# Optimization experiments

Measured on AMD Instinct MI355X. Metric: run time of the kernel, lower is better.

The kernel has to match this reference:

```python
import jax, jax.numpy as jnp
import numpy as np

# module constants (from init_kwargs)
CS, NV, ED = 8, 4, 32          # codebook_size, num_variables, embedding_dim
VIEWS, D, KSZ = 3, 16, 3        # num_input_channels, depth, kernel_size
HW = 14                         # 7 * scale (scale=2)
CSP = 8                         # spatial of conv_shape after three valid 3x3 convs: 14->12->10->8
KSTATES = CS ** NV              # 4096 combinatorial discrete states


def _elu(x):
    return jnp.where(x > 0, x, jnp.expm1(x))


def _conv_t(x, w, b):
    # PyTorch ConvTranspose2d(stride=1, padding=0); w: (Cin, Cout, k, k)
    wf = jnp.flip(w, (2, 3)).transpose(1, 0, 2, 3)  # -> (Cout, Cin, k, k)
    p = w.shape[2] - 1
    y = jax.lax.conv_general_dilated(x, wf, (1, 1), [(p, p), (p, p)],
                                     dimension_numbers=('NCHW', 'OIHW', 'NCHW'))
    return y + b[None, :, None, None]


def setup_inputs() -> dict:
    key = jax.random.key(0)
    ks = jax.random.split(key, 10)
    rn = lambda k, shape, s=1.0: jax.random.normal(k, shape, jnp.float32) * s
    return {
        'x': rn(ks[0], (64, VIEWS, HW, HW)),
        'latent_embedding': rn(ks[1], (NV, CS, ED)),
        'lin_w': rn(ks[2], (VIEWS, ED * NV, 4 * D * CSP * CSP), 0.05),
        'lin_b': rn(ks[3], (VIEWS, 4 * D * CSP * CSP), 0.05),
        'w1': rn(ks[4], (VIEWS, 4 * D, 2 * D, KSZ, KSZ), 0.05),
        'b1': rn(ks[5], (VIEWS, 2 * D), 0.05),
        'w2': rn(ks[6], (VIEWS, 2 * D, D, KSZ, KSZ), 0.05),
        'b2': rn(ks[7], (VIEWS, D), 0.05),
        'w3': rn(ks[8], (VIEWS, D, 1, KSZ, KSZ), 0.05),
        'b3': rn(ks[9], (VIEWS, 1), 0.05),
    }


def reference(x, latent_embedding, lin_w, lin_b, w1, b1, w2, b2, w3, b3):
    # all combinations of codebook indices (itertools.product order): [K, NV]
    all_idcs = jnp.stack(
        jnp.meshgrid(*([jnp.arange(CS)] * NV), indexing='ij'), -1).reshape(-1, NV)
    # gather: z[k, v, :] = latent_embedding[v, all_idcs[k, v], :]
    z = latent_embedding[jnp.arange(NV)[None, :], all_idcs]       # [K, NV, ED]
    zf = z.reshape(KSTATES, NV * ED)                              # 'b n d -> b (n d)'

    def decode(lw, lb, W1, B1, W2, B2, W3, B3):
        h = (zf @ lw + lb).reshape(KSTATES, 4 * D, CSP, CSP)
        h = _elu(_conv_t(h, W1, B1))
        h = _elu(_conv_t(h, W2, B2))
        h = _conv_t(h, W3, B3)
        return h[:, 0]                                            # [K, HW, HW]

    m = jax.vmap(decode)(lin_w, lin_b, w1, b1, w2, b2, w3, b3)    # [views, K, HW, HW]
    m = jnp.transpose(m, (1, 0, 2, 3))                            # [K, views, HW, HW]

    # obs_logits = -0.5 * sum_{h,w} (m[None] - x[:, None])**2, computed without
    # materializing the [B, K, views, HW, HW] broadcast tensor
    m2 = jnp.sum(m * m, axis=(-2, -1))                            # [K, views]
    x2 = jnp.sum(x * x, axis=(-2, -1))                            # [B, views]
    cross = jnp.einsum('kvhw,bvhw->bkv', m, x)                    # [B, K, views]
    return -0.5 * (m2[None] + x2[:, None] - 2.0 * cross)          # [B, K, views]
```

## Files before the change

### kernel.cpp

```cpp
#include <hip/hip_runtime.h>
#include <cstddef>


typedef __attribute__((ext_vector_type(4))) float f32x4;
typedef _Float16 half8v __attribute__((ext_vector_type(8)));
typedef _Float16 half4v __attribute__((ext_vector_type(4)));
typedef _Float16 half2v __attribute__((ext_vector_type(2)));

static __device__ __forceinline__ float elu(float s) {
    float e = __expf(s) - 1.0f;
    return s > 0.f ? s : e;
}
static __device__ __forceinline__ float dot2acc(int hpair, int wpair, float acc) {
#if __has_builtin(__builtin_amdgcn_fdot2)
    return __builtin_amdgcn_fdot2(__builtin_bit_cast(half2v, hpair),
                                  __builtin_bit_cast(half2v, wpair), acc, false);
#else
    half2v h = __builtin_bit_cast(half2v, hpair);
    half2v w = __builtin_bit_cast(half2v, wpair);
    acc = fmaf((float)h.x, (float)w.x, acc);
    return fmaf((float)h.y, (float)w.y, acc);
#endif
}
static __device__ __forceinline__ int sh2addr(int c, int r) {
    return c * 392 + r * 24 + (((r >> 2) & 3) << 3);
}

__global__ __launch_bounds__(320) void prep_kernel(const float* __restrict__ x,
                                                   const float* __restrict__ le,
                                                   const float* __restrict__ lin_w,
                                                   const float* __restrict__ lin_b,
                                                   const float* __restrict__ w1,
                                                   const float* __restrict__ b1,
                                                   const float* __restrict__ w2,
                                                   float* __restrict__ Qa,
                                                   float* __restrict__ Qb,
                                                   float* __restrict__ x2,
                                                   short* __restrict__ xB,
                                                   short* __restrict__ Wf) {
    int bid = blockIdx.x;
    int t = threadIdx.x;
    if (bid >= 198) {
        int pid = bid - 198;
        int v = pid % 3, part = pid / 3;
        if (part < 4) {
            int nb = part;
            short* xBv = xB + v * 14336 + nb * 3584;
            for (int idx = t; idx < 3584; idx += 320) {
                int j = idx & 7, lane = (idx >> 3) & 63, s = idx >> 9;
                int px = s * 32 + ((lane >> 4) << 3) + j;
                int b  = nb * 16 + (lane & 15);
                float val = (px < 196) ? x[(b * 3 + v) * 196 + px] : 0.f;
                _Float16 h = (_Float16)val;
                xBv[idx] = __builtin_bit_cast(short, h);
            }
        } else if (part == 4) {
            int w = t >> 6, lane = t & 63;
            for (int b = w; b < 64; b += 5) {
                const float* xp = x + (b * 3 + v) * 196;
                float s = 0.f;
                for (int px = lane; px < 196; px += 64) s = fmaf(xp[px], xp[px], s);
#pragma unroll
                for (int off = 32; off; off >>= 1) s += __shfl_down(s, off, 64);
                if (lane == 0) x2[v * 64 + b] = s;
            }
        } else if (t < 64) {
            int lane = t;
            const float* w2v = w2 + v * 32 * 16 * 9;
            int co = lane & 15;
            int cibase = (lane >> 4) * 8;
#pragma unroll
            for (int tap = 0; tap < 9; ++tap)
#pragma unroll
                for (int j = 0; j < 8; ++j) {
                    _Float16 h = (_Float16)w2v[((cibase + j) * 16 + co) * 9 + tap];
                    Wf[(((v * 9 + tap) * 64 + lane) << 3) + j] = __builtin_bit_cast(short, h);
                }
        }
        return;
    }
    __shared__ float sPt[64 * 144];
    __shared__ float sW[16 * 32 * 9];
    int row = bid % 33;
    int v   = (bid / 33) % 3;
    int z   = bid / 99;

    float pj[16];
    if (t < 256) {
        if (row < 32) {
            int vp = row >> 3;
            const float* base0 = lin_w + (size_t)v * 524288 + (size_t)vp * 131072 + t * 16;
            const float* lep = le + row * 32;
            f32x4 a0 = {0,0,0,0}, a1 = {0,0,0,0}, a2 = {0,0,0,0}, a3 = {0,0,0,0};
            for (int e = 0; e < 32; ++e) {
                float lv = lep[e];
                const float4* bp = (const float4*)(base0 + e * 4096);
                float4 b0 = bp[0], b1v_ = bp[1], b2v_ = bp[2], b3v_ = bp[3];
                a0[0] = fmaf(lv, b0.x, a0[0]);  a0[1] = fmaf(lv, b0.y, a0[1]);
                a0[2] = fmaf(lv, b0.z, a0[2]);  a0[3] = fmaf(lv, b0.w, a0[3]);
                a1[0] = fmaf(lv, b1v_.x, a1[0]); a1[1] = fmaf(lv, b1v_.y, a1[1]);
                a1[2] = fmaf(lv, b1v_.z, a1[2]); a1[3] = fmaf(lv, b1v_.w, a1[3]);
                a2[0] = fmaf(lv, b2v_.x, a2[0]); a2[1] = fmaf(lv, b2v_.y, a2[1]);
                a2[2] = fmaf(lv, b2v_.z, a2[2]); a2[3] = fmaf(lv, b2v_.w, a2[3]);
                a3[0] = fmaf(lv, b3v_.x, a3[0]); a3[1] = fmaf(lv, b3v_.y, a3[1]);
                a3[2] = fmaf(lv, b3v_.z, a3[2]); a3[3] = fmaf(lv, b3v_.w, a3[3]);
            }
#pragma unroll
            for (int j = 0; j < 4; ++j) {
                pj[j] = a0[j]; pj[4 + j] = a1[j]; pj[8 + j] = a2[j]; pj[12 + j] = a3[j];
            }
        } else {
            const float4* bp = (const float4*)(lin_b + v * 4096 + t * 16);
#pragma unroll
            for (int j = 0; j < 4; ++j) {
                float4 b = bp[j];
                pj[4 * j] = b.x; pj[4 * j + 1] = b.y; pj[4 * j + 2] = b.z; pj[4 * j + 3] = b.w;
            }
        }
    }
    float4* zp = (float4*)sPt;
    for (int i = t; i < 2304; i += 320) zp[i] = float4{0.f, 0.f, 0.f, 0.f};
    __syncthreads();
    if (t < 256) {
        int ci = t >> 2;
#pragma unroll
        for (int j = 0; j < 16; ++j) {
            int r = (t & 3) * 16 + j;
            int y = r >> 3, xx = r & 7;
            sPt[ci * 144 + (xx + 2) * 12 + (y + 2)] = pj[j];
        }
    }
    const float* w1v = w1 + (size_t)v * 18432;
    int co = t / 10, ox = t % 10;
    float acc[10];
#pragma unroll
    for (int i = 0; i < 10; ++i) acc[i] = 0.f;

    for (int c0 = z * 2; c0 < z * 2 + 2; ++c0) {
        __syncthreads();
        const float4* wsrc = (const float4*)(w1v + c0 * 4608);
        for (int i = t; i < 1152; i += 320) ((float4*)sW)[i] = wsrc[i];
        __syncthreads();
#pragma unroll 2
        for (int ci = 0; ci < 16; ++ci) {
            const float* xp = sPt + (c0 * 16 + ci) * 144;
            const float* wp = sW + (ci * 32 + co) * 9;
            float wv[9];
#pragma unroll
            for (int j = 0; j < 9; ++j) wv[j] = wp[j];
#pragma unroll
            for (int b = 0; b < 3; ++b) {
                const float* colp = xp + (ox + 2 - b) * 12;
                float4 c0v = *(const float4*)(colp);
                float4 c1v = *(const float4*)(colp + 4);
                float4 c2v = *(const float4*)(colp + 8);
                float cv[12] = {c0v.x, c0v.y, c0v.z, c0v.w,
                                c1v.x, c1v.y, c1v.z, c1v.w,
                                c2v.x, c2v.y, c2v.z, c2v.w};
#pragma unroll
                for (int a = 0; a < 3; ++a) {
                    float wgt = wv[a * 3 + b];
#pragma unroll
                    for (int oy = 0; oy < 10; ++oy)
                        acc[oy] = fmaf(cv[oy + 2 - a], wgt, acc[oy]);
                }
            }
        }
    }
    float bb = (z == 0 && row == 32) ? b1[v * 32 + co] : 0.f;
    float* dst = (z == 0 ? Qa : Qb) + (size_t)v * 105600 + row * 3200;
#pragma unroll
    for (int oy = 0; oy < 10; ++oy)
        dst[(ox * 10 + oy) * 32 + co] = acc[oy] + bb;
}

__global__ __launch_bounds__(256) void pair_kernel(const float* __restrict__ Qa,
                                                   const float* __restrict__ Qb,
                                                   float* __restrict__ Q01,
                                                   float* __restrict__ Q23b) {
    int p = blockIdx.x;
    int half = blockIdx.y;
    int v = blockIdx.z;
    const float4* basea = (const float4*)(Qa + (size_t)v * 105600);
    const float4* baseb = (const float4*)(Qb + (size_t)v * 105600);
    if (half == 0) {
        const float4* ra = basea + (p >> 3) * 800;
        const float4* rb = baseb + (p >> 3) * 800;
        const float4* rc = basea + (8 + (p & 7)) * 800;
        const float4* rd = baseb + (8 + (p & 7)) * 800;
        float4* dst = (float4*)(Q01 + (size_t)v * 204800 + p * 3200);
        for (int i = threadIdx.x; i < 800; i += 256) {
            float4 a = ra[i], b = rb[i], c = rc[i], d = rd[i];
            dst[i] = float4{a.x + b.x + c.x + d.x, a.y + b.y + c.y + d.y,
                            a.z + b.z + c.z + d.z, a.w + b.w + c.w + d.w};
        }
    } else {
        const float4* ra = basea + (16 + (p >> 3)) * 800;
        const float4* rb = baseb + (16 + (p >> 3)) * 800;
        const float4* rc = basea + (24 + (p & 7)) * 800;
        const float4* rd = baseb + (24 + (p & 7)) * 800;
        const float4* re = basea + 32 * 800;
        const float4* rf = baseb + 32 * 800;
        float4* dst = (float4*)(Q23b + (size_t)v * 204800 + p * 3200);
        for (int i = threadIdx.x; i < 800; i += 256) {
            float4 a = ra[i], b = rb[i], c = rc[i], d = rd[i], e = re[i], f = rf[i];
            dst[i] = float4{a.x + b.x + c.x + d.x + e.x + f.x,
                            a.y + b.y + c.y + d.y + e.y + f.y,
                            a.z + b.z + c.z + d.z + e.z + f.z,
                            a.w + b.w + c.w + d.w + e.w + f.w};
        }
    }
}

__global__ __launch_bounds__(256) void fusedgemm_kernel(const float* __restrict__ Q01,
                                                        const float* __restrict__ Q23b,
                                                        const short* __restrict__ Wf,
                                                        const float* __restrict__ b2,
                                                        const float* __restrict__ w3,
                                                        const float* __restrict__ b3,
                                                        const short* __restrict__ xB,
                                                        const float* __restrict__ x2g,
                                                        float* __restrict__ out) {
    __shared__ alignas(16) short sH1[196 * 40];
    __shared__ alignas(16) short sH2[6280];
    __shared__ alignas(16) short sM[16 * 224];
    __shared__ int sW3p[72];
    __shared__ float sM2[16];
    int k0 = blockIdx.x * 16;
    int v = blockIdx.y;
    int t = threadIdx.x;
    int lane = t & 63;
    int g = lane >> 4;
    int w = t >> 6;

    half8v bfrag[9];
#pragma unroll
    for (int tap = 0; tap < 9; ++tap)
        bfrag[tap] = *(const half8v*)(const void*)(Wf + (((v * 9 + tap) * 64 + lane) << 3));
    float bias2 = b2[v * 16 + (lane & 15)];
    float bias3 = b3[v];

    if (t < 16) sM2[t] = 0.f;
    for (int pix = t; pix < 196; pix += 256) {
        int c = pix / 14, r = pix % 14;
        if (c < 2 || c >= 12 || r < 2 || r >= 12) {
            int4* z = (int4*)(sH1 + pix * 40);
            z[0] = int4{0,0,0,0}; z[1] = int4{0,0,0,0};
            z[2] = int4{0,0,0,0}; z[3] = int4{0,0,0,0};
        }
    }
    {
        int c = t >> 4, r = t & 15;
        if (c < 2 || c >= 14 || r < 2 || r >= 14) {
            int4* z = (int4*)(sH2 + sh2addr(c, r));
            z[0] = int4{0,0,0,0}; z[1] = int4{0,0,0,0};
        }
    }
    if (t < 72) {
        int tap = t / 8, j = t % 8;
        half2v p = {(_Float16)w3[v * 144 + (2 * j) * 9 + tap],
                    (_Float16)w3[v * 144 + (2 * j + 1) * 9 + tap]};
        sW3p[t] = __builtin_bit_cast(int, p);
    }

    int st1[4]; bool v1[4];
    {
        int ci4 = (t & 7) * 4;
#pragma unroll
        for (int j = 0; j < 4; ++j) {
            int i = t + j * 256;
            v1[j] = (i < 800);
            int pix = i >> 3;
            int cx = pix / 10, ry = pix % 10;
            st1[j] = ((cx + 2) * 14 + (ry + 2)) * 40 + ci4;
        }
    }
    int ntile = 0; int bmoff[3]; int soff[3][4];
    for (int tile = w; tile < 9; tile += 4) {
        int m = tile * 16 + (lane & 15);
        int cx2 = m / 12, ry2 = m % 12;
        bmoff[ntile] = (cx2 * 14 + ry2) * 40 + g * 8;
        int p0 = tile * 16 + g * 4;
        int cxp = p0 / 12, ryp = p0 % 12;
        int co = lane & 15;
#pragma unroll
        for (int r = 0; r < 4; ++r) {
            soff[ntile][r] = sh2addr(cxp + 2, ryp + 2) + co;
            ++ryp; if (ryp == 12) { ryp = 0; ++cxp; }
        }
        ++ntile;
    }
    int off3[9];
    {
        int ry3 = (t < 196) ? t / 14 : 0;
        int cx3 = (t < 196) ? t % 14 : 0;
#pragma unroll
        for (int a = 0; a < 3; ++a)
#pragma unroll
            for (int b = 0; b < 3; ++b)
                off3[a * 3 + b] = sh2addr(cx3 + 2 - b, ry3 + 2 - a);
    }

    const float4* qa = (const float4*)(Q01 + ((size_t)v * 64 + (k0 >> 6)) * 3200);
    float4 ra[4];
    int kb = k0 & 63;

    for (int s = 0; s < 16; ++s) {
        {
            const float4* qb = (const float4*)(Q23b + ((size_t)v * 64 + (kb + s)) * 3200);
#pragma unroll
            for (int j = 0; j < 4; ++j) {
                if (v1[j]) {
                    int i = t + j * 256;
                    if (s == 0) ra[j] = qa[i];
                    float4 a = ra[j];
                    float4 b = qb[i];
                    half4v o = {(_Float16)elu(a.x + b.x), (_Float16)elu(a.y + b.y),
                                (_Float16)elu(a.z + b.z), (_Float16)elu(a.w + b.w)};
                    *(half4v*)(void*)(sH1 + st1[j]) = o;
                }
            }
        }
        __syncthreads();
#pragma unroll
        for (int it = 0; it < 3; ++it) {
            if (it < ntile) {
                const short* basemin = sH1 + bmoff[it];
                f32x4 acc0 = {bias2, bias2, bias2, bias2};
                f32x4 acc1 = {0.f, 0.f, 0.f, 0.f};
#pragma unroll
                for (int a = 0; a < 3; ++a)
#pragma unroll
                    for (int b = 0; b < 3; ++b) {
                        half8v af = *(const half8v*)(const void*)(basemin + ((2 - b) * 14 + (2 - a)) * 40);
                        int idx = a * 3 + b;
                        if (idx & 1)
                            acc1 = __builtin_amdgcn_mfma_f32_16x16x32_f16(af, bfrag[idx], acc1, 0, 0, 0);
                        else
                            acc0 = __builtin_amdgcn_mfma_f32_16x16x32_f16(af, bfrag[idx], acc0, 0, 0, 0);
                    }
#pragma unroll
                for (int r = 0; r < 4; ++r) {
                    _Float16 h = (_Float16)elu(acc0[r] + acc1[r]);
                    sH2[soff[it][r]] = __builtin_bit_cast(short, h);
                }
            }
        }
        __syncthreads();
        {
            float mval = 0.f;
            if (t < 196) {
                float a0 = bias3, a1 = 0.f, a2 = 0.f, a3 = 0.f;
#pragma unroll
                for (int tap = 0; tap < 9; ++tap) {
                    const short* base = sH2 + off3[tap];
                    int4 lo = *(const int4*)(const void*)(base);
                    int4 hi = *(const int4*)(const void*)(base + 8);
                    const int* wp = sW3p + tap * 8;
                    a0 = dot2acc(lo.x, wp[0], a0);
                    a1 = dot2acc(lo.y, wp[1], a1);
                    a2 = dot2acc(lo.z, wp[2], a2);
                    a3 = dot2acc(lo.w, wp[3], a3);
                    a0 = dot2acc(hi.x, wp[4], a0);
                    a1 = dot2acc(hi.y, wp[5], a1);
                    a2 = dot2acc(hi.z, wp[6], a2);
                    a3 = dot2acc(hi.w, wp[7], a3);
                }
                mval = (a0 + a1) + (a2 + a3);
            }
            if (t < 224) {
                _Float16 h = (_Float16)mval;
                sM[s * 224 + t] = __builtin_bit_cast(short, h);
            }
            float sq = mval * mval;
#pragma unroll
            for (int off = 32; off; off >>= 1) sq += __shfl_down(sq, off, 64);
            if (lane == 0) atomicAdd(&sM2[s], sq);
        }
    }
    __syncthreads();

    {
        f32x4 acc = {0.f, 0.f, 0.f, 0.f};
        const short* abase = sM + (lane & 15) * 224 + g * 8;
        const short* bbase = xB + (((v * 4 + w) * 7) * 64 + lane) * 8;
#pragma unroll
        for (int s7 = 0; s7 < 7; ++s7) {
            half8v af = *(const half8v*)(const void*)(abase + s7 * 32);
            half8v bf = *(const half8v*)(const void*)(bbase + s7 * 512);
            acc = __builtin_amdgcn_mfma_f32_16x16x32_f16(af, bf, acc, 0, 0, 0);
        }
        int b = w * 16 + (lane & 15);
        float x2v = x2g[v * 64 + b];
        size_t obase = ((size_t)b * 4096 + k0) * 3 + v;
#pragma unroll
        for (int r = 0; r < 4; ++r) {
            int kk = g * 4 + r;
            out[obase + (size_t)kk * 3] = acc[r] - 0.5f * (sM2[kk] + x2v);
        }
    }
}

extern "C" void kernel_launch(void* const* d_in, const int* in_sizes, int n_in,
                              void* d_out, int out_size, void* d_ws, size_t ws_size,
                              hipStream_t stream) {
    const float* x     = (const float*)d_in[0];
    const float* le    = (const float*)d_in[1];
    const float* lin_w = (const float*)d_in[2];
    const float* lin_b = (const float*)d_in[3];
    const float* w1    = (const float*)d_in[4];
    const float* b1    = (const float*)d_in[5];
    const float* w2    = (const float*)d_in[6];
    const float* b2    = (const float*)d_in[7];
    const float* w3    = (const float*)d_in[8];
    const float* b3    = (const float*)d_in[9];
    float* out = (float*)d_out;

    float* ws = (float*)d_ws;
    float* x2g  = ws;
    short* xB   = (short*)(ws + 192);
    short* Wf   = (short*)(ws + 21760);
    float* Qa   = ws + 28736;
    float* Qb   = ws + 345536;
    float* Q01  = ws + 662336;
    float* Q23b = ws + 1276736;

    prep_kernel<<<216, 320, 0, stream>>>(x, le, lin_w, lin_b, w1, b1, w2,
                                         Qa, Qb, x2g, xB, Wf);
    pair_kernel<<<dim3(64, 2, 3), 256, 0, stream>>>(Qa, Qb, Q01, Q23b);
    fusedgemm_kernel<<<dim3(256, 3), 256, 0, stream>>>(Q01, Q23b, Wf, b2, w3, b3,
                                                       xB, x2g, out);
}
```

Measured before the change: 175.0 us.

## Fuse pair-sum kernel into fused GEMM via shared-memory partial sums

Removes the separate pair_kernel, which materialised the Q01 and Q23b pairwise sums in global memory. The fused kernel now builds the sum of the first three variables' contributions plus bias in a new 12.8KB shared buffer every 8 states, then adds the fourth variable's contribution per state. This saves a kernel launch and a global write and read round trip. In exchange each block does more loads, adds a __syncthreads, and uses more LDS, which may lower occupancy.

```diff
diff --git a/kernel.cpp b/kernel.cpp
--- a/kernel.cpp
+++ b/kernel.cpp
@@ -174,46 +174,8 @@
         dst[(ox * 10 + oy) * 32 + co] = acc[oy] + bb;
 }
 
-__global__ __launch_bounds__(256) void pair_kernel(const float* __restrict__ Qa,
-                                                   const float* __restrict__ Qb,
-                                                   float* __restrict__ Q01,
-                                                   float* __restrict__ Q23b) {
-    int p = blockIdx.x;
-    int half = blockIdx.y;
-    int v = blockIdx.z;
-    const float4* basea = (const float4*)(Qa + (size_t)v * 105600);
-    const float4* baseb = (const float4*)(Qb + (size_t)v * 105600);
-    if (half == 0) {
-        const float4* ra = basea + (p >> 3) * 800;
-        const float4* rb = baseb + (p >> 3) * 800;
-        const float4* rc = basea + (8 + (p & 7)) * 800;
-        const float4* rd = baseb + (8 + (p & 7)) * 800;
-        float4* dst = (float4*)(Q01 + (size_t)v * 204800 + p * 3200);
-        for (int i = threadIdx.x; i < 800; i += 256) {
-            float4 a = ra[i], b = rb[i], c = rc[i], d = rd[i];
-            dst[i] = float4{a.x + b.x + c.x + d.x, a.y + b.y + c.y + d.y,
-                            a.z + b.z + c.z + d.z, a.w + b.w + c.w + d.w};
-        }
-    } else {
-        const float4* ra = basea + (16 + (p >> 3)) * 800;
-        const float4* rb = baseb + (16 + (p >> 3)) * 800;
-        const float4* rc = basea + (24 + (p & 7)) * 800;
-        const float4* rd = baseb + (24 + (p & 7)) * 800;
-        const float4* re = basea + 32 * 800;
-        const float4* rf = baseb + 32 * 800;
-        float4* dst = (float4*)(Q23b + (size_t)v * 204800 + p * 3200);
-        for (int i = threadIdx.x; i < 800; i += 256) {
-            float4 a = ra[i], b = rb[i], c = rc[i], d = rd[i], e = re[i], f = rf[i];
-            dst[i] = float4{a.x + b.x + c.x + d.x + e.x + f.x,
-                            a.y + b.y + c.y + d.y + e.y + f.y,
-                            a.z + b.z + c.z + d.z + e.z + f.z,
-                            a.w + b.w + c.w + d.w + e.w + f.w};
-        }
-    }
-}
-
-__global__ __launch_bounds__(256) void fusedgemm_kernel(const float* __restrict__ Q01,
-                                                        const float* __restrict__ Q23b,
+__global__ __launch_bounds__(256) void fusedgemm_kernel(const float* __restrict__ Qa,
+                                                        const float* __restrict__ Qb,
                                                         const short* __restrict__ Wf,
                                                         const float* __restrict__ b2,
                                                         const float* __restrict__ w3,
@@ -224,6 +186,7 @@
     __shared__ alignas(16) short sH1[196 * 40];
     __shared__ alignas(16) short sH2[6280];
     __shared__ alignas(16) short sM[16 * 224];
+    __shared__ alignas(16) float sQ[3200];
     __shared__ int sW3p[72];
     __shared__ float sM2[16];
     int k0 = blockIdx.x * 16;
@@ -301,22 +264,48 @@
                 off3[a * 3 + b] = sh2addr(cx3 + 2 - b, ry3 + 2 - a);
     }
 
-    const float4* qa = (const float4*)(Q01 + ((size_t)v * 64 + (k0 >> 6)) * 3200);
-    float4 ra[4];
-    int kb = k0 & 63;
+    const float* Qav = Qa + (size_t)v * 105600;
+    const float* Qbv = Qb + (size_t)v * 105600;
+    int i0 = (k0 >> 9) & 7;
+    int i1 = (k0 >> 6) & 7;
+    int i2b = (k0 >> 3) & 7;
 
     for (int s = 0; s < 16; ++s) {
+        if ((s & 7) == 0) {
+            int i2 = i2b + (s >> 3);
+            const float4* pa0 = (const float4*)(Qav + i0 * 3200);
+            const float4* pb0 = (const float4*)(Qbv + i0 * 3200);
+            const float4* pa1 = (const float4*)(Qav + (8 + i1) * 3200);
+            const float4* pb1 = (const float4*)(Qbv + (8 + i1) * 3200);
+            const float4* pa2 = (const float4*)(Qav + (16 + i2) * 3200);
+            const float4* pb2 = (const float4*)(Qbv + (16 + i2) * 3200);
+            const float4* pab = (const float4*)(Qav + 32 * 3200);
+            const float4* pbb = (const float4*)(Qbv + 32 * 3200);
+            float4* dq = (float4*)sQ;
+            for (int i = t; i < 800; i += 256) {
+                float4 A = pa0[i], B = pb0[i], C = pa1[i], D = pb1[i];
+                float4 E = pa2[i], F = pb2[i], G = pab[i], H = pbb[i];
+                dq[i] = float4{A.x + B.x + C.x + D.x + E.x + F.x + G.x + H.x,
+                               A.y + B.y + C.y + D.y + E.y + F.y + G.y + H.y,
+                               A.z + B.z + C.z + D.z + E.z + F.z + G.z + H.z,
+                               A.w + B.w + C.w + D.w + E.w + F.w + G.w + H.w};
+            }
+            __syncthreads();
+        }
         {
-            const float4* qb = (const float4*)(Q23b + ((size_t)v * 64 + (kb + s)) * 3200);
+            int i3 = s & 7;
+            const float4* qa3 = (const float4*)(Qav + (24 + i3) * 3200);
+            const float4* qb3 = (const float4*)(Qbv + (24 + i3) * 3200);
+            const float4* qs = (const float4*)sQ;
 #pragma unroll
             for (int j = 0; j < 4; ++j) {
                 if (v1[j]) {
                     int i = t + j * 256;
-                    if (s == 0) ra[j] = qa[i];
-                    float4 a = ra[j];
-                    float4 b = qb[i];
-                    half4v o = {(_Float16)elu(a.x + b.x), (_Float16)elu(a.y + b.y),
-                                (_Float16)elu(a.z + b.z), (_Float16)elu(a.w + b.w)};
+                    float4 q = qs[i], a = qa3[i], b = qb3[i];
+                    half4v o = {(_Float16)elu(q.x + a.x + b.x),
+                                (_Float16)elu(q.y + a.y + b.y),
+                                (_Float16)elu(q.z + a.z + b.z),
+                                (_Float16)elu(q.w + a.w + b.w)};
                     *(half4v*)(void*)(sH1 + st1[j]) = o;
                 }
             }
@@ -422,12 +411,9 @@
     short* Wf   = (short*)(ws + 21760);
     float* Qa   = ws + 28736;
     float* Qb   = ws + 345536;
-    float* Q01  = ws + 662336;
-    float* Q23b = ws + 1276736;
 
     prep_kernel<<<216, 320, 0, stream>>>(x, le, lin_w, lin_b, w1, b1, w2,
                                          Qa, Qb, x2g, xB, Wf);
-    pair_kernel<<<dim3(64, 2, 3), 256, 0, stream>>>(Qa, Qb, Q01, Q23b);
-    fusedgemm_kernel<<<dim3(256, 3), 256, 0, stream>>>(Q01, Q23b, Wf, b2, w3, b3,
+    fusedgemm_kernel<<<dim3(256, 3), 256, 0, stream>>>(Qa, Qb, Wf, b2, w3, b3,
                                                        xB, x2g, out);
 }
```

Result: no change. 173.8 us (-0.7%).

## Split linear projection into separate kernel and halve states per fused block

Applied to the files above, without the earlier changes.

Adds a pmat kernel that computes the per-codebook-entry linear projections (plus bias row) into a workspace buffer. The first-layer conv blocks then load only their half of the channels from that buffer instead of recomputing the projection redundantly. The fused conv/GEMM kernel now processes 8 states per block instead of 16, doubling the grid to 1536 blocks for better occupancy. The cost is an extra launch and workspace traffic, plus half of the MFMA rows being wasted (zero-filled) in the final product.

```diff
diff --git a/kernel.cpp b/kernel.cpp
--- a/kernel.cpp
+++ b/kernel.cpp
@@ -26,10 +26,36 @@
     return c * 392 + r * 24 + (((r >> 2) & 3) << 3);
 }
 
-__global__ __launch_bounds__(320) void prep_kernel(const float* __restrict__ x,
-                                                   const float* __restrict__ le,
+__global__ __launch_bounds__(256) void pmat_kernel(const float* __restrict__ le,
                                                    const float* __restrict__ lin_w,
                                                    const float* __restrict__ lin_b,
+                                                   float* __restrict__ P3) {
+    int o = blockIdx.x * 256 + threadIdx.x;
+    int y = blockIdx.y;
+    int v = blockIdx.z;
+    if (y == 4) {
+        P3[((size_t)v * 33 + 32) * 4096 + o] = lin_b[v * 4096 + o];
+        return;
+    }
+    int vp = y;
+    const float* lwv = lin_w + (size_t)v * 524288 + (size_t)vp * 131072 + o;
+    float acc[8];
+#pragma unroll
+    for (int j = 0; j < 8; ++j) acc[j] = 0.f;
+    const float* lep = le + vp * 8 * 32;
+    for (int e = 0; e < 32; ++e) {
+        float lw = lwv[e * 4096];
+#pragma unroll
+        for (int j = 0; j < 8; ++j)
+            acc[j] = fmaf(lep[j * 32 + e], lw, acc[j]);
+    }
+#pragma unroll
+    for (int j = 0; j < 8; ++j)
+        P3[((size_t)v * 33 + vp * 8 + j) * 4096 + o] = acc[j];
+}
+
+__global__ __launch_bounds__(320) void prep_kernel(const float* __restrict__ x,
+                                                   const float* __restrict__ P3,
                                                    const float* __restrict__ w1,
                                                    const float* __restrict__ b1,
                                                    const float* __restrict__ w2,
@@ -79,56 +105,19 @@
         }
         return;
     }
-    __shared__ float sPt[64 * 144];
+    __shared__ float sPt[32 * 144];
     __shared__ float sW[16 * 32 * 9];
     int row = bid % 33;
     int v   = (bid / 33) % 3;
     int z   = bid / 99;
 
-    float pj[16];
-    if (t < 256) {
-        if (row < 32) {
-            int vp = row >> 3;
-            const float* base0 = lin_w + (size_t)v * 524288 + (size_t)vp * 131072 + t * 16;
-            const float* lep = le + row * 32;
-            f32x4 a0 = {0,0,0,0}, a1 = {0,0,0,0}, a2 = {0,0,0,0}, a3 = {0,0,0,0};
-            for (int e = 0; e < 32; ++e) {
-                float lv = lep[e];
-                const float4* bp = (const float4*)(base0 + e * 4096);
-                float4 b0 = bp[0], b1v_ = bp[1], b2v_ = bp[2], b3v_ = bp[3];
-                a0[0] = fmaf(lv, b0.x, a0[0]);  a0[1] = fmaf(lv, b0.y, a0[1]);
-                a0[2] = fmaf(lv, b0.z, a0[2]);  a0[3] = fmaf(lv, b0.w, a0[3]);
-                a1[0] = fmaf(lv, b1v_.x, a1[0]); a1[1] = fmaf(lv, b1v_.y, a1[1]);
-                a1[2] = fmaf(lv, b1v_.z, a1[2]); a1[3] = fmaf(lv, b1v_.w, a1[3]);
-                a2[0] = fmaf(lv, b2v_.x, a2[0]); a2[1] = fmaf(lv, b2v_.y, a2[1]);
-                a2[2] = fmaf(lv, b2v_.z, a2[2]); a2[3] = fmaf(lv, b2v_.w, a2[3]);
-                a3[0] = fmaf(lv, b3v_.x, a3[0]); a3[1] = fmaf(lv, b3v_.y, a3[1]);
-                a3[2] = fmaf(lv, b3v_.z, a3[2]); a3[3] = fmaf(lv, b3v_.w, a3[3]);
-            }
-#pragma unroll
-            for (int j = 0; j < 4; ++j) {
-                pj[j] = a0[j]; pj[4 + j] = a1[j]; pj[8 + j] = a2[j]; pj[12 + j] = a3[j];
-            }
-        } else {
-            const float4* bp = (const float4*)(lin_b + v * 4096 + t * 16);
-#pragma unroll
-            for (int j = 0; j < 4; ++j) {
-                float4 b = bp[j];
-                pj[4 * j] = b.x; pj[4 * j + 1] = b.y; pj[4 * j + 2] = b.z; pj[4 * j + 3] = b.w;
-            }
-        }
-    }
+    const float* src = P3 + ((size_t)v * 33 + row) * 4096 + z * 2048;
     float4* zp = (float4*)sPt;
-    for (int i = t; i < 2304; i += 320) zp[i] = float4{0.f, 0.f, 0.f, 0.f};
+    for (int i = t; i < 1152; i += 320) zp[i] = float4{0.f, 0.f, 0.f, 0.f};
     __syncthreads();
-    if (t < 256) {
-        int ci = t >> 2;
-#pragma unroll
-        for (int j = 0; j < 16; ++j) {
-            int r = (t & 3) * 16 + j;
-            int y = r >> 3, xx = r & 7;
-            sPt[ci * 144 + (xx + 2) * 12 + (y + 2)] = pj[j];
-        }
+    for (int i = t; i < 2048; i += 320) {
+        int ci = i >> 6, r = i & 63, y = r >> 3, xx = r & 7;
+        sPt[ci * 144 + (xx + 2) * 12 + (y + 2)] = src[i];
     }
     const float* w1v = w1 + (size_t)v * 18432;
     int co = t / 10, ox = t % 10;
@@ -136,14 +125,15 @@
 #pragma unroll
     for (int i = 0; i < 10; ++i) acc[i] = 0.f;
 
-    for (int c0 = z * 2; c0 < z * 2 + 2; ++c0) {
+    for (int c0l = 0; c0l < 2; ++c0l) {
+        int c0 = z * 2 + c0l;
         __syncthreads();
         const float4* wsrc = (const float4*)(w1v + c0 * 4608);
         for (int i = t; i < 1152; i += 320) ((float4*)sW)[i] = wsrc[i];
         __syncthreads();
 #pragma unroll 2
         for (int ci = 0; ci < 16; ++ci) {
-            const float* xp = sPt + (c0 * 16 + ci) * 144;
+            const float* xp = sPt + (c0l * 16 + ci) * 144;
             const float* wp = sW + (ci * 32 + co) * 9;
             float wv[9];
 #pragma unroll
@@ -223,10 +213,10 @@
                                                         float* __restrict__ out) {
     __shared__ alignas(16) short sH1[196 * 40];
     __shared__ alignas(16) short sH2[6280];
-    __shared__ alignas(16) short sM[16 * 224];
+    __shared__ alignas(16) short sM[8 * 224];
     __shared__ int sW3p[72];
-    __shared__ float sM2[16];
-    int k0 = blockIdx.x * 16;
+    __shared__ float sM2[8];
+    int k0 = blockIdx.x * 8;
     int v = blockIdx.y;
     int t = threadIdx.x;
     int lane = t & 63;
@@ -240,7 +230,7 @@
     float bias2 = b2[v * 16 + (lane & 15)];
     float bias3 = b3[v];
 
-    if (t < 16) sM2[t] = 0.f;
+    if (t < 8) sM2[t] = 0.f;
     for (int pix = t; pix < 196; pix += 256) {
         int c = pix / 14, r = pix % 14;
         if (c < 2 || c >= 12 || r < 2 || r >= 12) {
@@ -305,7 +295,7 @@
     float4 ra[4];
     int kb = k0 & 63;
 
-    for (int s = 0; s < 16; ++s) {
+    for (int s = 0; s < 8; ++s) {
         {
             const float4* qb = (const float4*)(Q23b + ((size_t)v * 64 + (kb + s)) * 3200);
 #pragma unroll
@@ -382,21 +372,24 @@
 
     {
         f32x4 acc = {0.f, 0.f, 0.f, 0.f};
-        const short* abase = sM + (lane & 15) * 224 + g * 8;
+        int mrow = lane & 15;
+        const short* abase = sM + mrow * 224 + g * 8;
         const short* bbase = xB + (((v * 4 + w) * 7) * 64 + lane) * 8;
+        half8v zero8 = {0, 0, 0, 0, 0, 0, 0, 0};
 #pragma unroll
         for (int s7 = 0; s7 < 7; ++s7) {
-            half8v af = *(const half8v*)(const void*)(abase + s7 * 32);
+            half8v af = (mrow < 8) ? *(const half8v*)(const void*)(abase + s7 * 32) : zero8;
             half8v bf = *(const half8v*)(const void*)(bbase + s7 * 512);
             acc = __builtin_amdgcn_mfma_f32_16x16x32_f16(af, bf, acc, 0, 0, 0);
         }
-        int b = w * 16 + (lane & 15);
+        int b = w * 16 + mrow;
         float x2v = x2g[v * 64 + b];
         size_t obase = ((size_t)b * 4096 + k0) * 3 + v;
 #pragma unroll
         for (int r = 0; r < 4; ++r) {
             int kk = g * 4 + r;
-            out[obase + (size_t)kk * 3] = acc[r] - 0.5f * (sM2[kk] + x2v);
+            if (kk < 8)
+                out[obase + (size_t)kk * 3] = acc[r] - 0.5f * (sM2[kk] + x2v);
         }
     }
 }
@@ -422,12 +415,13 @@
     short* Wf   = (short*)(ws + 21760);
     float* Qa   = ws + 28736;
     float* Qb   = ws + 345536;
-    float* Q01  = ws + 662336;
-    float* Q23b = ws + 1276736;
-
-    prep_kernel<<<216, 320, 0, stream>>>(x, le, lin_w, lin_b, w1, b1, w2,
-                                         Qa, Qb, x2g, xB, Wf);
+    float* P3   = ws + 662336;
+    float* Q01  = ws + 1067840;
+    float* Q23b = ws + 1682240;
+
+    pmat_kernel<<<dim3(16, 5, 3), 256, 0, stream>>>(le, lin_w, lin_b, P3);
+    prep_kernel<<<216, 320, 0, stream>>>(x, P3, w1, b1, w2, Qa, Qb, x2g, xB, Wf);
     pair_kernel<<<dim3(64, 2, 3), 256, 0, stream>>>(Qa, Qb, Q01, Q23b);
-    fusedgemm_kernel<<<dim3(256, 3), 256, 0, stream>>>(Q01, Q23b, Wf, b2, w3, b3,
+    fusedgemm_kernel<<<dim3(512, 3), 256, 0, stream>>>(Q01, Q23b, Wf, b2, w3, b3,
                                                        xB, x2g, out);
 }
```

Measured after the change: 176.3 us. No clear change (+0.8%).
